# Kernel tuning notes

Hardware: AMD Instinct MI355X
Metric: run time of the kernel (lower is better)

The kernel has to match this reference:

```python
import jax, jax.numpy as jnp
import numpy as np

D = 768      # hidden_size
H = 12       # num_attention_heads
HD = D // H  # head_dim = 64
L = 12       # num_hidden_layers (same head weights reused every layer)


def setup_inputs() -> dict:
    key = jax.random.key(0)
    ks = jax.random.split(key, 9)
    s_in = 1.0 / np.sqrt(D)
    s_hd = 1.0 / np.sqrt(HD)
    x = jax.random.normal(ks[0], (8, 1024, D), dtype=jnp.float32)
    # Per-head weights stacked on a leading head axis.
    Wq = jax.random.normal(ks[1], (H, D, HD), dtype=jnp.float32) * s_in
    Wk = jax.random.normal(ks[2], (H, D, HD), dtype=jnp.float32) * s_in
    Wv = jax.random.normal(ks[3], (H, D, HD), dtype=jnp.float32) * s_in
    Wo = jax.random.normal(ks[4], (H, HD, HD), dtype=jnp.float32) * s_hd
    bq = jax.random.normal(ks[5], (H, HD), dtype=jnp.float32) * 0.02
    bk = jax.random.normal(ks[6], (H, HD), dtype=jnp.float32) * 0.02
    bv = jax.random.normal(ks[7], (H, HD), dtype=jnp.float32) * 0.02
    bo = jax.random.normal(ks[8], (H, HD), dtype=jnp.float32) * 0.02
    return {"x": x, "Wq": Wq, "bq": bq, "Wk": Wk, "bk": bk,
            "Wv": Wv, "bv": bv, "Wo": Wo, "bo": bo}


def _mha_layer(x, Wq, bq, Wk, bk, Wv, bv, Wo, bo):
    B, S, _ = x.shape
    # per-head projections: [B,H,S,HD]
    q = jnp.einsum('bsd,hdk->bhsk', x, Wq) + bq[None, :, None, :]
    k = jnp.einsum('bsd,hdk->bhsk', x, Wk) + bk[None, :, None, :]
    v = jnp.einsum('bsd,hdk->bhsk', x, Wv) + bv[None, :, None, :]
    scores = jnp.einsum('bhsk,bhtk->bhst', q, k) / jnp.sqrt(jnp.float32(HD))
    attn = jax.nn.softmax(scores, axis=-1)
    ctx = jnp.einsum('bhst,bhtk->bhsk', attn, v)
    # per-head output linear (head_dim -> head_dim), then concat over heads
    out = jnp.einsum('bhsk,hkm->bhsm', ctx, Wo) + bo[None, :, None, :]
    return out.transpose(0, 2, 1, 3).reshape(B, S, D)


def reference(x, Wq, bq, Wk, bk, Wv, bv, Wo, bo):
    # The module applies the SAME set of head weights num_hidden_layers times.
    for _ in range(L):
        x = _mha_layer(x, Wq, bq, Wk, bk, Wv, bv, Wo, bo)
    return x
```

## Files before the change

### kernel.cpp

```cpp
#include <hip/hip_runtime.h>

#define NB 8
#define NS 1024
#define ND 768
#define NH 12
#define NHD 64
#define NLAYERS 12
#define NM (NB * NS)
#define NQKV3 (3 * ND)
#define QSCALE 0.1803368802f

typedef _Float16 f16;
typedef _Float16 f16x8 __attribute__((ext_vector_type(8)));
typedef _Float16 f16x4 __attribute__((ext_vector_type(4)));
typedef _Float16 f16x2 __attribute__((ext_vector_type(2)));
typedef float f32x4 __attribute__((ext_vector_type(4)));
typedef float f32x16 __attribute__((ext_vector_type(16)));
typedef unsigned int u32x4 __attribute__((ext_vector_type(4)));

__device__ inline float fexp2(float x) {
  float r;
  asm("v_exp_f32 %0, %1" : "=v"(r) : "v"(x));
  return r;
}

__device__ __forceinline__ void gload16(const void* g, void* l) {
  __builtin_amdgcn_global_load_lds(
      (const __attribute__((address_space(1))) void*)g,
      (__attribute__((address_space(3))) void*)l, 16, 0, 0);
}

__global__ __launch_bounds__(256) void prep_weights(
    const float* __restrict__ Wq, const float* __restrict__ Wk,
    const float* __restrict__ Wv, const float* __restrict__ Wo,
    const float* __restrict__ bv, const float* __restrict__ bo,
    f16* __restrict__ Wcat, float* __restrict__ bvo) {
  __shared__ float t0[64][65];
  __shared__ float t1[64 * 64];
  int bid = blockIdx.x, tid = threadIdx.x;
  if (bid < 288) {
    int dt = bid % 12, hh = (bid / 12) % 12, sel = bid / 144;
    const float* W = sel == 0 ? Wq : Wk;
    int d0 = dt * 64;
#pragma unroll
    for (int p = 0; p < 16; ++p) {
      int i = p * 4 + (tid >> 6), kp = tid & 63;
      t0[i][kp] = W[(size_t)(hh * 768 + d0 + i) * 64 + kp];
    }
    __syncthreads();
#pragma unroll
    for (int p = 0; p < 16; ++p) {
      int kp = p * 4 + (tid >> 6), i = tid & 63;
      Wcat[(size_t)(sel * 768 + hh * 64 + kp) * 768 + d0 + i] = (f16)t0[i][kp];
    }
  } else if (bid < 432) {
    int idx = bid - 288, hh = idx / 12, dt = idx % 12, d0 = dt * 64;
#pragma unroll
    for (int p = 0; p < 16; ++p) {
      int i = p * 4 + (tid >> 6), m = tid & 63;
      t0[i][m] = Wv[(size_t)(hh * 768 + d0 + i) * 64 + m];
      t1[i * 64 + m] = Wo[(size_t)(hh * 64 + i) * 64 + m];
    }
    __syncthreads();
    int j = tid & 63;
    for (int p = 0; p < 16; ++p) {
      int i = p * 4 + (tid >> 6);
      float a = 0.f;
      for (int m = 0; m < 64; ++m) a += t0[i][m] * t1[m * 64 + j];
      Wcat[(size_t)(1536 + hh * 64 + j) * 768 + d0 + i] = (f16)a;
    }
  } else {
    for (int base = 0; base < 768; base += 256) {
      int idx = base + tid, h2 = idx >> 6, j = idx & 63;
      float a = bo[idx];
      for (int m = 0; m < 64; ++m)
        a += bv[h2 * 64 + m] * Wo[(size_t)(h2 * 64 + m) * 64 + j];
      bvo[idx] = a;
    }
  }
}

__global__ __launch_bounds__(256) void x_to_f16(const float* __restrict__ x,
                                                f16* __restrict__ xh) {
  size_t i = (size_t)blockIdx.x * 256 + threadIdx.x;
  float4 v = reinterpret_cast<const float4*>(x)[i];
  f16x4 o;
  o[0] = (f16)v.x; o[1] = (f16)v.y; o[2] = (f16)v.z; o[3] = (f16)v.w;
  reinterpret_cast<f16x4*>(xh)[i] = o;
}

#define QK_AS (128 * 32)
#define QK_BS (192 * 32)
__global__ __launch_bounds__(256, 3) void qkv_gemm(
    const f16* __restrict__ Xh, const f16* __restrict__ Wcat,
    const float* __restrict__ bq, const float* __restrict__ bk,
    f16* __restrict__ Qo, f16* __restrict__ Ko, f16* __restrict__ Vto) {
  __shared__ __align__(16) f16 SH[2 * QK_AS + 2 * QK_BS];
  int tid = threadIdx.x, lane = tid & 63, wid = tid >> 6;
  int l16 = lane & 15, g4 = lane >> 4;
  int r0 = blockIdx.x * 128, n0 = blockIdx.y * 192;
  int wm = wid & 1, wn = wid >> 1;
  f32x4 acc[4][6] = {};

  const f16* gA[2];
  const f16* gB[3];
  int la[2], lb[3];
#pragma unroll
  for (int ss = 0; ss < 2; ++ss) {
    int s = ss * 256 + tid, row = s >> 2, cs = s & 3;
    int csrc = cs ^ ((row >> 1) & 3);
    gA[ss] = Xh + (size_t)(r0 + row) * 768 + csrc * 8;
    la[ss] = s * 16;
  }
#pragma unroll
  for (int ss = 0; ss < 3; ++ss) {
    int s = ss * 256 + tid, row = s >> 2, cs = s & 3;
    int csrc = cs ^ ((row >> 1) & 3);
    gB[ss] = Wcat + (size_t)(n0 + row) * 768 + csrc * 8;
    lb[ss] = s * 16;
  }
  auto stage = [&](int buf, int kk) {
    char* A = (char*)(SH + buf * QK_AS);
    char* B = (char*)(SH + 2 * QK_AS + buf * QK_BS);
#pragma unroll
    for (int ss = 0; ss < 2; ++ss) gload16(gA[ss] + kk, A + la[ss]);
#pragma unroll
    for (int ss = 0; ss < 3; ++ss) gload16(gB[ss] + kk, B + lb[ss]);
  };
  auto compute = [&](int buf) {
    const f16* A = SH + buf * QK_AS;
    const f16* B = SH + 2 * QK_AS + buf * QK_BS;
    f16x8 af[4], bf[6];
#pragma unroll
    for (int mf = 0; mf < 4; ++mf) {
      int row = wm * 64 + mf * 16 + l16;
      int ch = g4 ^ ((row >> 1) & 3);
      af[mf] = *(const f16x8*)(A + row * 32 + ch * 8);
    }
#pragma unroll
    for (int nf = 0; nf < 6; ++nf) {
      int row = wn * 96 + nf * 16 + l16;
      int ch = g4 ^ ((row >> 1) & 3);
      bf[nf] = *(const f16x8*)(B + row * 32 + ch * 8);
    }
#pragma unroll
    for (int mf = 0; mf < 4; ++mf)
#pragma unroll
      for (int nf = 0; nf < 6; ++nf)
        acc[mf][nf] = __builtin_amdgcn_mfma_f32_16x16x32_f16(af[mf], bf[nf],
                                                             acc[mf][nf], 0, 0, 0);
  };

  stage(0, 0);
  __syncthreads();
  int cur = 0;
  for (int kk = 0; kk < 768; kk += 32) {
    bool more = kk + 32 < 768;
    if (more) stage(cur ^ 1, kk + 32);
    compute(cur);
    if (more) {
      __syncthreads();
      cur ^= 1;
    }
  }

  int sel = n0 / 768;
  int nrem = n0 % 768;
  __syncthreads();
  if (sel < 2) {
    const float* bp = sel == 0 ? bq : bk;
    float scl = sel == 0 ? QSCALE : 1.f;
    f16* dst = sel == 0 ? Qo : Ko;
#pragma unroll
    for (int rh = 0; rh < 2; ++rh) {
      if (wm == rh) {
#pragma unroll
        for (int nf = 0; nf < 6; ++nf) {
          int c = wn * 96 + nf * 16 + l16;
          float bia = bp[nrem + c];
#pragma unroll
          for (int mf = 0; mf < 4; ++mf)
#pragma unroll
            for (int r = 0; r < 4; ++r)
              SH[(mf * 16 + g4 * 4 + r) * 208 + c] =
                  (f16)((acc[mf][nf][r] + bia) * scl);
        }
      }
      __syncthreads();
#pragma unroll
      for (int p = 0; p < 6; ++p) {
        int cl = p * 256 + tid;
        int lr = cl / 24, ch = cl % 24;
        int grow = r0 + rh * 64 + lr;
        int b = grow >> 10, s = grow & 1023;
        int col = nrem + ch * 8;
        int hh = col >> 6, kp = col & 63;
        f16x8 v = *(const f16x8*)(SH + lr * 208 + ch * 8);
        *(f16x8*)(dst + ((size_t)(b * 12 + hh) * 1024 + s) * 64 + kp) = v;
      }
      __syncthreads();
    }
  } else {
#pragma unroll
    for (int rh = 0; rh < 2; ++rh) {
      if (wm == rh) {
#pragma unroll
        for (int nf = 0; nf < 6; ++nf) {
          int c = wn * 96 + nf * 16 + l16;
#pragma unroll
          for (int mf = 0; mf < 4; ++mf)
#pragma unroll
            for (int r = 0; r < 4; ++r)
              SH[c * 72 + mf * 16 + g4 * 4 + r] = (f16)acc[mf][nf][r];
        }
      }
      __syncthreads();
      int grow0 = r0 + rh * 64;
      int b = grow0 >> 10, s0 = grow0 & 1023;
#pragma unroll
      for (int p = 0; p < 6; ++p) {
        int cl = p * 256 + tid;
        int c = cl >> 3, ch = cl & 7;
        int col = nrem + c;
        int hh = col >> 6, kp = col & 63;
        f16x8 v = *(const f16x8*)(SH + c * 72 + ch * 8);
        *(f16x8*)(Vto + ((size_t)(b * 12 + hh) * 64 + kp) * 1024 + s0 + ch * 8) = v;
      }
      __syncthreads();
    }
  }
}

struct SMemKV { f16 K[2][64 * 64]; f16 V[2][64 * 64]; };
union SMemU { SMemKV kv; float O[4 * 32 * 68]; };

__global__ __launch_bounds__(256, 3) void attn_fused(
    const f16* __restrict__ Qg, const f16* __restrict__ Kg,
    const f16* __restrict__ Vt, const float* __restrict__ bvo,
    f16* __restrict__ XhOut, float* __restrict__ Fout, int last) {
  __shared__ __align__(16) SMemU sm;
  int tid = threadIdx.x, lane = tid & 63, wid = tid >> 6;
  int l32 = lane & 31, hi = lane >> 5;
  int lin = blockIdx.x;
  int qb = lin / 96;
  int hb = lin % 96;
  int hh = hb % 12, bb = hb / 12;
  int q0 = qb * 128;
  size_t bh = (size_t)bb * 12 + hh;
  const f16* Qp = Qg + bh * (1024 * 64);
  const f16* Kp = Kg + bh * (1024 * 64);
  const f16* Vp = Vt + bh * (64 * 1024);

  f16x8 qf[4];
#pragma unroll
  for (int kf = 0; kf < 4; ++kf)
    qf[kf] = *(const f16x8*)(Qp + (size_t)(q0 + wid * 32 + l32) * 64 + kf * 16 + hi * 8);

  f16x8 rk[2], rv[2];
  auto kv_load = [&](int t0) {
#pragma unroll
    for (int ss = 0; ss < 2; ++ss) {
      int cl = ss * 256 + tid, r = cl >> 3, c = cl & 7;
      rk[ss] = *(const f16x8*)(Kp + (size_t)(t0 + r) * 64 + c * 8);
      rv[ss] = *(const f16x8*)(Vp + (size_t)r * 1024 + t0 + c * 8);
    }
  };
  auto kv_store = [&](int buf) {
#pragma unroll
    for (int ss = 0; ss < 2; ++ss) {
      int cl = ss * 256 + tid, r = cl >> 3, c = cl & 7;
      int cs = c ^ (r & 7);
      *(f16x8*)(sm.kv.K[buf] + r * 64 + cs * 8) = rk[ss];
      *(f16x8*)(sm.kv.V[buf] + r * 64 + cs * 8) = rv[ss];
    }
  };

  f32x16 oacc0 = {}, oacc1 = {};
  float m = -1e30f, lsum = 0.f;

  kv_load(0);
  kv_store(0);
  __syncthreads();
  int cur = 0;
  for (int t = 0; t < 16; ++t) {
    bool more = t < 15;
    if (more) kv_load((t + 1) * 64);
    const f16* Kc = sm.kv.K[cur];
    const f16* Vc = sm.kv.V[cur];
    f32x16 sc0 = {}, sc1 = {};
#pragma unroll
    for (int kf = 0; kf < 4; ++kf) {
      int ch = (2 * kf + hi) ^ (l32 & 7);
      f16x8 k0 = *(const f16x8*)(Kc + l32 * 64 + ch * 8);
      sc0 = __builtin_amdgcn_mfma_f32_32x32x16_f16(k0, qf[kf], sc0, 0, 0, 0);
      f16x8 k1 = *(const f16x8*)(Kc + (32 + l32) * 64 + ch * 8);
      sc1 = __builtin_amdgcn_mfma_f32_32x32x16_f16(k1, qf[kf], sc1, 0, 0, 0);
    }
    float mx[16];
#pragma unroll
    for (int j = 0; j < 16; ++j) mx[j] = fmaxf(sc0[j], sc1[j]);
#pragma unroll
    for (int s = 8; s >= 1; s >>= 1)
#pragma unroll
      for (int j = 0; j < 8; ++j)
        if (j < s) mx[j] = fmaxf(mx[j], mx[j + s]);
    float pmax = fmaxf(mx[0], __shfl_xor(mx[0], 32));
    if (__any(pmax > m + 8.f)) {
      float mn = fmaxf(m, pmax);
      float c = fexp2(m - mn);
      lsum *= c;
#pragma unroll
      for (int j = 0; j < 16; ++j) { oacc0[j] *= c; oacc1[j] *= c; }
      m = mn;
    }
    unsigned w[8][2];
    float qs[8];
#pragma unroll
    for (int qd = 0; qd < 8; ++qd) {
      float a0, a1, a2, a3;
      if (qd < 4) {
        a0 = fexp2(sc0[qd * 4 + 0] - m); a1 = fexp2(sc0[qd * 4 + 1] - m);
        a2 = fexp2(sc0[qd * 4 + 2] - m); a3 = fexp2(sc0[qd * 4 + 3] - m);
      } else {
        a0 = fexp2(sc1[(qd - 4) * 4 + 0] - m); a1 = fexp2(sc1[(qd - 4) * 4 + 1] - m);
        a2 = fexp2(sc1[(qd - 4) * 4 + 2] - m); a3 = fexp2(sc1[(qd - 4) * 4 + 3] - m);
      }
      qs[qd] = (a0 + a1) + (a2 + a3);
      w[qd][0] = __builtin_bit_cast(unsigned, __builtin_amdgcn_cvt_pkrtz(a0, a1));
      w[qd][1] = __builtin_bit_cast(unsigned, __builtin_amdgcn_cvt_pkrtz(a2, a3));
    }
    lsum += ((qs[0] + qs[1]) + (qs[2] + qs[3])) + ((qs[4] + qs[5]) + (qs[6] + qs[7]));
#pragma unroll
    for (int kf = 0; kf < 4; ++kf) {
      int QB = (kf >> 1) * 4 + 2 * (kf & 1);
      unsigned lo0, lo1, hi0, hi1;
      {
        unsigned s0 = hi ? w[QB][0] : w[QB + 1][0];
        unsigned s1 = hi ? w[QB][1] : w[QB + 1][1];
        unsigned r0 = __shfl_xor(s0, 32);
        unsigned r1 = __shfl_xor(s1, 32);
        lo0 = hi ? r0 : w[QB][0];
        lo1 = hi ? r1 : w[QB][1];
        hi0 = hi ? w[QB + 1][0] : r0;
        hi1 = hi ? w[QB + 1][1] : r1;
      }
      u32x4 pw = {lo0, lo1, hi0, hi1};
      f16x8 pf = __builtin_bit_cast(f16x8, pw);
      int ch = (2 * kf + hi) ^ (l32 & 7);
      f16x8 v0 = *(const f16x8*)(Vc + l32 * 64 + ch * 8);
      oacc0 = __builtin_amdgcn_mfma_f32_32x32x16_f16(v0, pf, oacc0, 0, 0, 0);
      f16x8 v1 = *(const f16x8*)(Vc + (32 + l32) * 64 + ch * 8);
      oacc1 = __builtin_amdgcn_mfma_f32_32x32x16_f16(v1, pf, oacc1, 0, 0, 0);
    }
    if (more) {
      kv_store(cur ^ 1);
      __syncthreads();
      cur ^= 1;
    }
  }
  float lt = lsum + __shfl_xor(lsum, 32);
  float inv = 1.f / lt;
  __syncthreads();
  float* Ow = sm.O + wid * (32 * 68) + l32 * 68;
#pragma unroll
  for (int dt = 0; dt < 2; ++dt) {
#pragma unroll
    for (int g = 0; g < 4; ++g) {
      int d0 = dt * 32 + g * 8 + hi * 4;
      f32x4 st;
      if (dt == 0) {
        st[0] = oacc0[g * 4 + 0] * inv; st[1] = oacc0[g * 4 + 1] * inv;
        st[2] = oacc0[g * 4 + 2] * inv; st[3] = oacc0[g * 4 + 3] * inv;
      } else {
        st[0] = oacc1[g * 4 + 0] * inv; st[1] = oacc1[g * 4 + 1] * inv;
        st[2] = oacc1[g * 4 + 2] * inv; st[3] = oacc1[g * 4 + 3] * inv;
      }
      *(f32x4*)(Ow + d0) = st;
    }
  }
  __syncthreads();
  int base_q = bb * 1024 + q0;
#pragma unroll
  for (int p = 0; p < 8; ++p) {
    int cl = p * 256 + tid;
    int row = cl >> 4, c = cl & 15;
    f32x4 v = *(const f32x4*)(sm.O + (row >> 5) * (32 * 68) + (row & 31) * 68 + c * 4);
    float4 bv4 = *(const float4*)(bvo + hh * 64 + c * 4);
    v[0] += bv4.x; v[1] += bv4.y; v[2] += bv4.z; v[3] += bv4.w;
    size_t off = (size_t)(base_q + row) * 768 + hh * 64 + c * 4;
    if (last) {
      *(f32x4*)(Fout + off) = v;
    } else {
      f16x4 hq;
      hq[0] = (f16)v[0]; hq[1] = (f16)v[1]; hq[2] = (f16)v[2]; hq[3] = (f16)v[3];
      *(f16x4*)(XhOut + off) = hq;
    }
  }
}

extern "C" void kernel_launch(void* const* d_in, const int* in_sizes, int n_in,
                              void* d_out, int out_size, void* d_ws,
                              size_t ws_size, hipStream_t stream) {
  const float* x = (const float*)d_in[0];
  const float* Wq = (const float*)d_in[1];
  const float* bq = (const float*)d_in[2];
  const float* Wk = (const float*)d_in[3];
  const float* bk = (const float*)d_in[4];
  const float* Wv = (const float*)d_in[5];
  const float* bv = (const float*)d_in[6];
  const float* Wo = (const float*)d_in[7];
  const float* bo = (const float*)d_in[8];
  float* out = (float*)d_out;

  char* ws = (char*)d_ws;
  size_t off = 0;
  auto alloc = [&](size_t bytes) -> void* {
    void* p = ws + off;
    off += (bytes + 255) & ~(size_t)255;
    return p;
  };
  f16* Wcat = (f16*)alloc((size_t)NQKV3 * ND * 2);
  float* bvo = (float*)alloc(768 * 4);
  f16* Xh = (f16*)alloc((size_t)NM * ND * 2);
  f16* Qb = (f16*)alloc((size_t)NM * ND * 2);
  f16* Kb = (f16*)alloc((size_t)NM * ND * 2);
  f16* Vtb = (f16*)alloc((size_t)NM * ND * 2);

  prep_weights<<<433, 256, 0, stream>>>(Wq, Wk, Wv, Wo, bv, bo, Wcat, bvo);
  x_to_f16<<<(NM * ND / 4) / 256, 256, 0, stream>>>(x, Xh);
  for (int l = 0; l < NLAYERS; ++l) {
    qkv_gemm<<<dim3(NM / 128, NQKV3 / 192), 256, 0, stream>>>(
        Xh, Wcat, bq, bk, Qb, Kb, Vtb);
    attn_fused<<<768, 256, 0, stream>>>(
        Qb, Kb, Vtb, bvo, Xh, out, l == NLAYERS - 1);
  }
}
```

Measured before the change: 943.0 us.

## Give each attention wave two query subtiles and load K/V straight into LDS

The attention block shrinks from 4 waves to 2, and each wave now handles 64 query rows as two 32-row subtiles. Every K and V fragment read from LDS then feeds two MFMAs, which roughly halves LDS traffic per unit of math. K/V staging changes from global-to-register-then-LDS copies to direct global-to-LDS loads (gload16), with the XOR swizzle applied on the source address. The trade-off is more registers per wave and fewer waves per workgroup, which can lower occupancy and latency hiding.

```diff
diff --git a/kernel.cpp b/kernel.cpp
--- a/kernel.cpp
+++ b/kernel.cpp
@@ -232,9 +232,9 @@
 }
 
 struct SMemKV { f16 K[2][64 * 64]; f16 V[2][64 * 64]; };
-union SMemU { SMemKV kv; float O[4 * 32 * 68]; };
-
-__global__ __launch_bounds__(256, 3) void attn_fused(
+union SMemU { SMemKV kv; float O[128 * 68]; };
+
+__global__ __launch_bounds__(128, 2) void attn_fused(
     const f16* __restrict__ Qg, const f16* __restrict__ Kg,
     const f16* __restrict__ Vt, const float* __restrict__ bvo,
     f16* __restrict__ XhOut, float* __restrict__ Fout, int last) {
@@ -251,140 +251,160 @@
   const f16* Kp = Kg + bh * (1024 * 64);
   const f16* Vp = Vt + bh * (64 * 1024);
 
-  f16x8 qf[4];
-#pragma unroll
-  for (int kf = 0; kf < 4; ++kf)
-    qf[kf] = *(const f16x8*)(Qp + (size_t)(q0 + wid * 32 + l32) * 64 + kf * 16 + hi * 8);
-
-  f16x8 rk[2], rv[2];
-  auto kv_load = [&](int t0) {
-#pragma unroll
-    for (int ss = 0; ss < 2; ++ss) {
-      int cl = ss * 256 + tid, r = cl >> 3, c = cl & 7;
-      rk[ss] = *(const f16x8*)(Kp + (size_t)(t0 + r) * 64 + c * 8);
-      rv[ss] = *(const f16x8*)(Vp + (size_t)r * 1024 + t0 + c * 8);
+  f16x8 qf[2][4];
+#pragma unroll
+  for (int s = 0; s < 2; ++s)
+#pragma unroll
+    for (int kf = 0; kf < 4; ++kf)
+      qf[s][kf] = *(const f16x8*)(Qp + (size_t)(q0 + wid * 64 + s * 32 + l32) * 64 +
+                                  kf * 16 + hi * 8);
+
+  const f16* gK[4];
+  const f16* gV[4];
+  int lofs[4];
+#pragma unroll
+  for (int ss = 0; ss < 4; ++ss) {
+    int s = ss * 128 + tid, r = s >> 3, cs = s & 7;
+    int csrc = cs ^ (r & 7);
+    gK[ss] = Kp + r * 64 + csrc * 8;
+    gV[ss] = Vp + (size_t)r * 1024 + csrc * 8;
+    lofs[ss] = s * 16;
+  }
+  auto stage = [&](int buf, int t0) {
+    char* K = (char*)sm.kv.K[buf];
+    char* V = (char*)sm.kv.V[buf];
+#pragma unroll
+    for (int ss = 0; ss < 4; ++ss) {
+      gload16(gK[ss] + t0 * 64, K + lofs[ss]);
+      gload16(gV[ss] + t0, V + lofs[ss]);
     }
   };
-  auto kv_store = [&](int buf) {
-#pragma unroll
-    for (int ss = 0; ss < 2; ++ss) {
-      int cl = ss * 256 + tid, r = cl >> 3, c = cl & 7;
-      int cs = c ^ (r & 7);
-      *(f16x8*)(sm.kv.K[buf] + r * 64 + cs * 8) = rk[ss];
-      *(f16x8*)(sm.kv.V[buf] + r * 64 + cs * 8) = rv[ss];
-    }
-  };
-
-  f32x16 oacc0 = {}, oacc1 = {};
-  float m = -1e30f, lsum = 0.f;
-
-  kv_load(0);
-  kv_store(0);
+
+  f32x16 oacc[2][2] = {};
+  float m[2] = {-1e30f, -1e30f}, lsum[2] = {0.f, 0.f};
+
+  stage(0, 0);
   __syncthreads();
   int cur = 0;
   for (int t = 0; t < 16; ++t) {
     bool more = t < 15;
-    if (more) kv_load((t + 1) * 64);
+    if (more) stage(cur ^ 1, (t + 1) * 64);
     const f16* Kc = sm.kv.K[cur];
     const f16* Vc = sm.kv.V[cur];
-    f32x16 sc0 = {}, sc1 = {};
+    f32x16 sc[2][2] = {};
 #pragma unroll
     for (int kf = 0; kf < 4; ++kf) {
       int ch = (2 * kf + hi) ^ (l32 & 7);
       f16x8 k0 = *(const f16x8*)(Kc + l32 * 64 + ch * 8);
-      sc0 = __builtin_amdgcn_mfma_f32_32x32x16_f16(k0, qf[kf], sc0, 0, 0, 0);
       f16x8 k1 = *(const f16x8*)(Kc + (32 + l32) * 64 + ch * 8);
-      sc1 = __builtin_amdgcn_mfma_f32_32x32x16_f16(k1, qf[kf], sc1, 0, 0, 0);
-    }
-    float mx[16];
-#pragma unroll
-    for (int j = 0; j < 16; ++j) mx[j] = fmaxf(sc0[j], sc1[j]);
-#pragma unroll
-    for (int s = 8; s >= 1; s >>= 1)
-#pragma unroll
-      for (int j = 0; j < 8; ++j)
-        if (j < s) mx[j] = fmaxf(mx[j], mx[j + s]);
-    float pmax = fmaxf(mx[0], __shfl_xor(mx[0], 32));
-    if (__any(pmax > m + 8.f)) {
-      float mn = fmaxf(m, pmax);
-      float c = fexp2(m - mn);
-      lsum *= c;
-#pragma unroll
-      for (int j = 0; j < 16; ++j) { oacc0[j] *= c; oacc1[j] *= c; }
-      m = mn;
-    }
-    unsigned w[8][2];
-    float qs[8];
-#pragma unroll
-    for (int qd = 0; qd < 8; ++qd) {
-      float a0, a1, a2, a3;
-      if (qd < 4) {
-        a0 = fexp2(sc0[qd * 4 + 0] - m); a1 = fexp2(sc0[qd * 4 + 1] - m);
-        a2 = fexp2(sc0[qd * 4 + 2] - m); a3 = fexp2(sc0[qd * 4 + 3] - m);
-      } else {
-        a0 = fexp2(sc1[(qd - 4) * 4 + 0] - m); a1 = fexp2(sc1[(qd - 4) * 4 + 1] - m);
-        a2 = fexp2(sc1[(qd - 4) * 4 + 2] - m); a3 = fexp2(sc1[(qd - 4) * 4 + 3] - m);
-      }
-      qs[qd] = (a0 + a1) + (a2 + a3);
-      w[qd][0] = __builtin_bit_cast(unsigned, __builtin_amdgcn_cvt_pkrtz(a0, a1));
-      w[qd][1] = __builtin_bit_cast(unsigned, __builtin_amdgcn_cvt_pkrtz(a2, a3));
-    }
-    lsum += ((qs[0] + qs[1]) + (qs[2] + qs[3])) + ((qs[4] + qs[5]) + (qs[6] + qs[7]));
+#pragma unroll
+      for (int s = 0; s < 2; ++s) {
+        sc[s][0] = __builtin_amdgcn_mfma_f32_32x32x16_f16(k0, qf[s][kf], sc[s][0], 0, 0, 0);
+        sc[s][1] = __builtin_amdgcn_mfma_f32_32x32x16_f16(k1, qf[s][kf], sc[s][1], 0, 0, 0);
+      }
+    }
+    float pm[2];
+#pragma unroll
+    for (int s = 0; s < 2; ++s) {
+      float mx[16];
+#pragma unroll
+      for (int j = 0; j < 16; ++j) mx[j] = fmaxf(sc[s][0][j], sc[s][1][j]);
+#pragma unroll
+      for (int st = 8; st >= 1; st >>= 1)
+#pragma unroll
+        for (int j = 0; j < 8; ++j)
+          if (j < st) mx[j] = fmaxf(mx[j], mx[j + st]);
+      pm[s] = fmaxf(mx[0], __shfl_xor(mx[0], 32));
+    }
+    if (__any(fmaxf(pm[0] - m[0], pm[1] - m[1]) > 8.f)) {
+#pragma unroll
+      for (int s = 0; s < 2; ++s) {
+        float mn = fmaxf(m[s], pm[s]);
+        float c = fexp2(m[s] - mn);
+        lsum[s] *= c;
+#pragma unroll
+        for (int j = 0; j < 16; ++j) { oacc[s][0][j] *= c; oacc[s][1][j] *= c; }
+        m[s] = mn;
+      }
+    }
+    unsigned w[2][8][2];
+#pragma unroll
+    for (int s = 0; s < 2; ++s) {
+      float qs[8];
+#pragma unroll
+      for (int qd = 0; qd < 8; ++qd) {
+        float a0, a1, a2, a3;
+        if (qd < 4) {
+          a0 = fexp2(sc[s][0][qd * 4 + 0] - m[s]); a1 = fexp2(sc[s][0][qd * 4 + 1] - m[s]);
+          a2 = fexp2(sc[s][0][qd * 4 + 2] - m[s]); a3 = fexp2(sc[s][0][qd * 4 + 3] - m[s]);
+        } else {
+          a0 = fexp2(sc[s][1][(qd - 4) * 4 + 0] - m[s]); a1 = fexp2(sc[s][1][(qd - 4) * 4 + 1] - m[s]);
+          a2 = fexp2(sc[s][1][(qd - 4) * 4 + 2] - m[s]); a3 = fexp2(sc[s][1][(qd - 4) * 4 + 3] - m[s]);
+        }
+        qs[qd] = (a0 + a1) + (a2 + a3);
+        w[s][qd][0] = __builtin_bit_cast(unsigned, __builtin_amdgcn_cvt_pkrtz(a0, a1));
+        w[s][qd][1] = __builtin_bit_cast(unsigned, __builtin_amdgcn_cvt_pkrtz(a2, a3));
+      }
+      lsum[s] += ((qs[0] + qs[1]) + (qs[2] + qs[3])) + ((qs[4] + qs[5]) + (qs[6] + qs[7]));
+    }
 #pragma unroll
     for (int kf = 0; kf < 4; ++kf) {
       int QB = (kf >> 1) * 4 + 2 * (kf & 1);
-      unsigned lo0, lo1, hi0, hi1;
-      {
-        unsigned s0 = hi ? w[QB][0] : w[QB + 1][0];
-        unsigned s1 = hi ? w[QB][1] : w[QB + 1][1];
+      int ch = (2 * kf + hi) ^ (l32 & 7);
+      f16x8 v0 = *(const f16x8*)(Vc + l32 * 64 + ch * 8);
+      f16x8 v1 = *(const f16x8*)(Vc + (32 + l32) * 64 + ch * 8);
+#pragma unroll
+      for (int s = 0; s < 2; ++s) {
+        unsigned s0 = hi ? w[s][QB][0] : w[s][QB + 1][0];
+        unsigned s1 = hi ? w[s][QB][1] : w[s][QB + 1][1];
         unsigned r0 = __shfl_xor(s0, 32);
         unsigned r1 = __shfl_xor(s1, 32);
-        lo0 = hi ? r0 : w[QB][0];
-        lo1 = hi ? r1 : w[QB][1];
-        hi0 = hi ? w[QB + 1][0] : r0;
-        hi1 = hi ? w[QB + 1][1] : r1;
-      }
-      u32x4 pw = {lo0, lo1, hi0, hi1};
-      f16x8 pf = __builtin_bit_cast(f16x8, pw);
-      int ch = (2 * kf + hi) ^ (l32 & 7);
-      f16x8 v0 = *(const f16x8*)(Vc + l32 * 64 + ch * 8);
-      oacc0 = __builtin_amdgcn_mfma_f32_32x32x16_f16(v0, pf, oacc0, 0, 0, 0);
-      f16x8 v1 = *(const f16x8*)(Vc + (32 + l32) * 64 + ch * 8);
-      oacc1 = __builtin_amdgcn_mfma_f32_32x32x16_f16(v1, pf, oacc1, 0, 0, 0);
+        unsigned lo0 = hi ? r0 : w[s][QB][0];
+        unsigned lo1 = hi ? r1 : w[s][QB][1];
+        unsigned hi0 = hi ? w[s][QB + 1][0] : r0;
+        unsigned hi1 = hi ? w[s][QB + 1][1] : r1;
+        u32x4 pw = {lo0, lo1, hi0, hi1};
+        f16x8 pf = __builtin_bit_cast(f16x8, pw);
+        oacc[s][0] = __builtin_amdgcn_mfma_f32_32x32x16_f16(v0, pf, oacc[s][0], 0, 0, 0);
+        oacc[s][1] = __builtin_amdgcn_mfma_f32_32x32x16_f16(v1, pf, oacc[s][1], 0, 0, 0);
+      }
     }
     if (more) {
-      kv_store(cur ^ 1);
       __syncthreads();
       cur ^= 1;
     }
   }
-  float lt = lsum + __shfl_xor(lsum, 32);
-  float inv = 1.f / lt;
+  float inv[2];
+#pragma unroll
+  for (int s = 0; s < 2; ++s) {
+    float lt = lsum[s] + __shfl_xor(lsum[s], 32);
+    inv[s] = 1.f / lt;
+  }
   __syncthreads();
-  float* Ow = sm.O + wid * (32 * 68) + l32 * 68;
-#pragma unroll
-  for (int dt = 0; dt < 2; ++dt) {
-#pragma unroll
-    for (int g = 0; g < 4; ++g) {
-      int d0 = dt * 32 + g * 8 + hi * 4;
-      f32x4 st;
-      if (dt == 0) {
-        st[0] = oacc0[g * 4 + 0] * inv; st[1] = oacc0[g * 4 + 1] * inv;
-        st[2] = oacc0[g * 4 + 2] * inv; st[3] = oacc0[g * 4 + 3] * inv;
-      } else {
-        st[0] = oacc1[g * 4 + 0] * inv; st[1] = oacc1[g * 4 + 1] * inv;
-        st[2] = oacc1[g * 4 + 2] * inv; st[3] = oacc1[g * 4 + 3] * inv;
-      }
-      *(f32x4*)(Ow + d0) = st;
+#pragma unroll
+  for (int s = 0; s < 2; ++s) {
+    float* Ow = sm.O + (size_t)(wid * 64 + s * 32 + l32) * 68;
+#pragma unroll
+    for (int dt = 0; dt < 2; ++dt) {
+#pragma unroll
+      for (int g = 0; g < 4; ++g) {
+        int d0 = dt * 32 + g * 8 + hi * 4;
+        f32x4 st;
+        st[0] = oacc[s][dt][g * 4 + 0] * inv[s];
+        st[1] = oacc[s][dt][g * 4 + 1] * inv[s];
+        st[2] = oacc[s][dt][g * 4 + 2] * inv[s];
+        st[3] = oacc[s][dt][g * 4 + 3] * inv[s];
+        *(f32x4*)(Ow + d0) = st;
+      }
     }
   }
   __syncthreads();
   int base_q = bb * 1024 + q0;
 #pragma unroll
-  for (int p = 0; p < 8; ++p) {
-    int cl = p * 256 + tid;
+  for (int p = 0; p < 16; ++p) {
+    int cl = p * 128 + tid;
     int row = cl >> 4, c = cl & 15;
-    f32x4 v = *(const f32x4*)(sm.O + (row >> 5) * (32 * 68) + (row & 31) * 68 + c * 4);
+    f32x4 v = *(const f32x4*)(sm.O + row * 68 + c * 4);
     float4 bv4 = *(const float4*)(bvo + hh * 64 + c * 4);
     v[0] += bv4.x; v[1] += bv4.y; v[2] += bv4.z; v[3] += bv4.w;
     size_t off = (size_t)(base_q + row) * 768 + hh * 64 + c * 4;
@@ -431,7 +451,7 @@
   for (int l = 0; l < NLAYERS; ++l) {
     qkv_gemm<<<dim3(NM / 128, NQKV3 / 192), 256, 0, stream>>>(
         Xh, Wcat, bq, bk, Qb, Kb, Vtb);
-    attn_fused<<<768, 256, 0, stream>>>(
+    attn_fused<<<768, 128, 0, stream>>>(
         Qb, Kb, Vtb, bvo, Xh, out, l == NLAYERS - 1);
   }
 }
```

Result: slower. 970.7 us, median of 2 (+2.9%).
